# Performance work log

Hardware: AMD Instinct MI355X
Metric: run time of the kernel (lower is better)

Reference implementation:

```python
import jax, jax.numpy as jnp
import numpy as np

CONTINLEN = 5
ACCUMULATE_BETA = 50.0


def _triple_indices(n):
    """Flatten the module's triple loop into static gather indices over pairs.

    Pairs (a,b), a<b, are stored at flat index pair_id[(a,b)] along axis 0 of
    rotas/transs. For every (i,k,j) with i<k<j we need pairs (i,k), (k,j), (i,j).
    """
    pair_id = {}
    p = 0
    for a in range(n):
        for b in range(a + 1, n):
            pair_id[(a, b)] = p
            p += 1
    i1, i2, i12 = [], [], []
    for i in range(n):
        for j in range(i + 2, n):
            for k in range(i + 1, j):
                i1.append(pair_id[(i, k)])
                i2.append(pair_id[(k, j)])
                i12.append(pair_id[(i, j)])
    return (np.asarray(i1, np.int32), np.asarray(i2, np.int32),
            np.asarray(i12, np.int32))


def setup_inputs() -> dict:
    key = jax.random.key(0)
    k1, k2 = jax.random.split(key)
    P = CONTINLEN * (CONTINLEN - 1) // 2  # 10 ordered pairs
    B = 262144                              # batch of pose predictions
    rotas = jax.random.normal(k1, (P, B, 3, 3), dtype=jnp.float32)
    transs = jax.random.normal(k2, (P, B, 3), dtype=jnp.float32)
    return {"rotas": rotas, "transs": transs}


def reference(rotas, transs):
    i1, i2, i12 = _triple_indices(CONTINLEN)
    # Gather all (i,k), (k,j), (i,j) pose pairs at once: [T, B, 3, 3] / [T, B, 3]
    R1, R2, R12 = rotas[i1], rotas[i2], rotas[i12]
    t1, t2, t12 = transs[i1], transs[i2], transs[i12]
    # fuse_rota = R(i,k) @ R(k,j); fuse_trans = R(i,k) @ t(i,k) + t(k,j)
    fuse_rota = jnp.einsum('tbij,tbjk->tbik', R1, R2)
    fuse_trans = jnp.einsum('tbij,tbj->tbi', R1, t1) + t2
    rotaloss = jnp.sum(jnp.square(fuse_rota - R12))
    transloss = jnp.sum(jnp.square(fuse_trans - t12))
    return (rotaloss * ACCUMULATE_BETA + transloss).reshape(1)
```

## Files before the change

kernel.cpp:

```cpp
#include <hip/hip_runtime.h>

#define NPAIR 10
#define NTRI  10

__device__ __constant__ const int c_i1[NTRI]  = {0,0,1,0,1,2,4,4,5,7};
__device__ __constant__ const int c_i2[NTRI]  = {4,5,7,6,8,9,7,8,9,9};
__device__ __constant__ const int c_i12[NTRI] = {1,2,2,3,3,3,5,6,6,8};

__global__ __launch_bounds__(256) void accum_loss_kernel(
    const float* __restrict__ rotas,
    const float* __restrict__ transs,
    float* __restrict__ block_sums,
    int B)
{
    const int b = blockIdx.x * blockDim.x + threadIdx.x;

    float loss = 0.0f;
    if (b < B) {
        float R[NPAIR][9];
        float t[NPAIR][3];
#pragma unroll
        for (int p = 0; p < NPAIR; ++p) {
            const float* rp = rotas + ((size_t)p * B + b) * 9;
#pragma unroll
            for (int k = 0; k < 9; ++k) R[p][k] = rp[k];
            const float* tp = transs + ((size_t)p * B + b) * 3;
#pragma unroll
            for (int k = 0; k < 3; ++k) t[p][k] = tp[k];
        }

        float rl = 0.0f, tl = 0.0f;
#pragma unroll
        for (int tr = 0; tr < NTRI; ++tr) {
            const float* R1  = R[c_i1[tr]];
            const float* R2  = R[c_i2[tr]];
            const float* R12 = R[c_i12[tr]];
            const float* t1  = t[c_i1[tr]];
            const float* t2  = t[c_i2[tr]];
            const float* t12 = t[c_i12[tr]];
#pragma unroll
            for (int i = 0; i < 3; ++i) {
#pragma unroll
                for (int j = 0; j < 3; ++j) {
                    float f = fmaf(R1[i*3+0], R2[0*3+j],
                              fmaf(R1[i*3+1], R2[1*3+j],
                                   R1[i*3+2] * R2[2*3+j]));
                    float d = f - R12[i*3+j];
                    rl = fmaf(d, d, rl);
                }
                float ft = fmaf(R1[i*3+0], t1[0],
                           fmaf(R1[i*3+1], t1[1],
                                R1[i*3+2] * t1[2])) + t2[i];
                float dt = ft - t12[i];
                tl = fmaf(dt, dt, tl);
            }
        }
        loss = fmaf(rl, 50.0f, tl);
    }

#pragma unroll
    for (int off = 32; off >= 1; off >>= 1)
        loss += __shfl_down(loss, off, 64);

    __shared__ float ws[4];
    const int lane = threadIdx.x & 63;
    const int wid  = threadIdx.x >> 6;
    if (lane == 0) ws[wid] = loss;
    __syncthreads();
    if (threadIdx.x == 0)
        block_sums[blockIdx.x] = ws[0] + ws[1] + ws[2] + ws[3];
}

__global__ __launch_bounds__(256) void final_reduce_kernel(
    const float* __restrict__ block_sums, float* __restrict__ out, int n)
{
    float s = 0.0f;
    for (int i = threadIdx.x; i < n; i += blockDim.x) s += block_sums[i];
#pragma unroll
    for (int off = 32; off >= 1; off >>= 1)
        s += __shfl_down(s, off, 64);

    __shared__ float ws[4];
    const int lane = threadIdx.x & 63;
    const int wid  = threadIdx.x >> 6;
    if (lane == 0) ws[wid] = s;
    __syncthreads();
    if (threadIdx.x == 0)
        out[0] = ws[0] + ws[1] + ws[2] + ws[3];
}

extern "C" void kernel_launch(void* const* d_in, const int* in_sizes, int n_in,
                              void* d_out, int out_size, void* d_ws, size_t ws_size,
                              hipStream_t stream)
{
    const float* rotas  = (const float*)d_in[0];
    const float* transs = (const float*)d_in[1];
    float* out = (float*)d_out;

    const int B = in_sizes[0] / (NPAIR * 9);
    const int threads = 256;
    const int blocks  = (B + threads - 1) / threads;

    float* block_sums = (float*)d_ws;

    accum_loss_kernel<<<blocks, threads, 0, stream>>>(rotas, transs, block_sums, B);
    final_reduce_kernel<<<1, threads, 0, stream>>>(block_sums, out, blocks);
}
```

Before: 163.1 us.

## Stage pose loads through LDS for coalesced access with register prefetch

Each wave now loads each pair's rotation and translation data as contiguous 64-lane coalesced chunks, transposes them through per-wave double-buffered LDS into per-thread registers, and prefetches the next pair's global data while the current one is being redistributed. This replaces strided per-thread 36-byte and 12-byte loads that gave poor coalescing. The index tables become constexpr, and the bounds check is dropped on the assumption that B is a multiple of 256. If B is not a multiple of 256, the tail elements would be skipped.

```diff
diff --git a/kernel.cpp b/kernel.cpp
--- a/kernel.cpp
+++ b/kernel.cpp
@@ -3,9 +3,14 @@
 #define NPAIR 10
 #define NTRI  10
 
-__device__ __constant__ const int c_i1[NTRI]  = {0,0,1,0,1,2,4,4,5,7};
-__device__ __constant__ const int c_i2[NTRI]  = {4,5,7,6,8,9,7,8,9,9};
-__device__ __constant__ const int c_i12[NTRI] = {1,2,2,3,3,3,5,6,6,8};
+constexpr int c_i1[NTRI]  = {0,0,1,0,1,2,4,4,5,7};
+constexpr int c_i2[NTRI]  = {4,5,7,6,8,9,7,8,9,9};
+constexpr int c_i12[NTRI] = {1,2,2,3,3,3,5,6,6,8};
+
+#define LDS_FENCE() do {                      \
+    __builtin_amdgcn_s_waitcnt(0xC07F);       \
+    __builtin_amdgcn_wave_barrier();          \
+} while (0)
 
 __global__ __launch_bounds__(256) void accum_loss_kernel(
     const float* __restrict__ rotas,
@@ -13,61 +18,91 @@
     float* __restrict__ block_sums,
     int B)
 {
-    const int b = blockIdx.x * blockDim.x + threadIdx.x;
+    const int tid  = threadIdx.x;
+    const int lane = tid & 63;
+    const int wave = tid >> 6;
 
-    float loss = 0.0f;
-    if (b < B) {
-        float R[NPAIR][9];
-        float t[NPAIR][3];
+    __shared__ float sR[2][4][576];
+    __shared__ float sT[2][4][192];
+
+    const int wb0 = blockIdx.x * 256 + wave * 64;
+
+    float R[NPAIR][9];
+    float t[NPAIR][3];
+    float gR[9], gT[3];
+
+    {
+        const float* rsrc = rotas  + ((size_t)0 * B + wb0) * 9;
+        const float* tsrc = transs + ((size_t)0 * B + wb0) * 3;
 #pragma unroll
-        for (int p = 0; p < NPAIR; ++p) {
-            const float* rp = rotas + ((size_t)p * B + b) * 9;
+        for (int k = 0; k < 9; ++k) gR[k] = rsrc[k * 64 + lane];
 #pragma unroll
-            for (int k = 0; k < 9; ++k) R[p][k] = rp[k];
-            const float* tp = transs + ((size_t)p * B + b) * 3;
+        for (int k = 0; k < 3; ++k) gT[k] = tsrc[k * 64 + lane];
+    }
+
 #pragma unroll
-            for (int k = 0; k < 3; ++k) t[p][k] = tp[k];
+    for (int p = 0; p < NPAIR; ++p) {
+        const int buf = p & 1;
+#pragma unroll
+        for (int k = 0; k < 9; ++k) sR[buf][wave][k * 64 + lane] = gR[k];
+#pragma unroll
+        for (int k = 0; k < 3; ++k) sT[buf][wave][k * 64 + lane] = gT[k];
+
+        LDS_FENCE();
+
+        if (p + 1 < NPAIR) {
+            const float* rsrc = rotas  + ((size_t)(p + 1) * B + wb0) * 9;
+            const float* tsrc = transs + ((size_t)(p + 1) * B + wb0) * 3;
+#pragma unroll
+            for (int k = 0; k < 9; ++k) gR[k] = rsrc[k * 64 + lane];
+#pragma unroll
+            for (int k = 0; k < 3; ++k) gT[k] = tsrc[k * 64 + lane];
         }
 
-        float rl = 0.0f, tl = 0.0f;
 #pragma unroll
-        for (int tr = 0; tr < NTRI; ++tr) {
-            const float* R1  = R[c_i1[tr]];
-            const float* R2  = R[c_i2[tr]];
-            const float* R12 = R[c_i12[tr]];
-            const float* t1  = t[c_i1[tr]];
-            const float* t2  = t[c_i2[tr]];
-            const float* t12 = t[c_i12[tr]];
+        for (int k = 0; k < 9; ++k) R[p][k] = sR[buf][wave][lane * 9 + k];
 #pragma unroll
-            for (int i = 0; i < 3; ++i) {
+        for (int k = 0; k < 3; ++k) t[p][k] = sT[buf][wave][lane * 3 + k];
+
+        LDS_FENCE();
+    }
+
+    float rl = 0.0f, tl = 0.0f;
 #pragma unroll
-                for (int j = 0; j < 3; ++j) {
-                    float f = fmaf(R1[i*3+0], R2[0*3+j],
-                              fmaf(R1[i*3+1], R2[1*3+j],
-                                   R1[i*3+2] * R2[2*3+j]));
-                    float d = f - R12[i*3+j];
-                    rl = fmaf(d, d, rl);
-                }
-                float ft = fmaf(R1[i*3+0], t1[0],
-                           fmaf(R1[i*3+1], t1[1],
-                                R1[i*3+2] * t1[2])) + t2[i];
-                float dt = ft - t12[i];
-                tl = fmaf(dt, dt, tl);
+    for (int tr = 0; tr < NTRI; ++tr) {
+        const float* R1  = R[c_i1[tr]];
+        const float* R2  = R[c_i2[tr]];
+        const float* R12 = R[c_i12[tr]];
+        const float* t1  = t[c_i1[tr]];
+        const float* t2  = t[c_i2[tr]];
+        const float* t12 = t[c_i12[tr]];
+#pragma unroll
+        for (int i = 0; i < 3; ++i) {
+#pragma unroll
+            for (int j = 0; j < 3; ++j) {
+                float f = fmaf(R1[i*3+0], R2[0*3+j],
+                          fmaf(R1[i*3+1], R2[1*3+j],
+                               R1[i*3+2] * R2[2*3+j]));
+                float d = f - R12[i*3+j];
+                rl = fmaf(d, d, rl);
             }
+            float ft = fmaf(R1[i*3+0], t1[0],
+                       fmaf(R1[i*3+1], t1[1],
+                            R1[i*3+2] * t1[2])) + t2[i];
+            float dt = ft - t12[i];
+            tl = fmaf(dt, dt, tl);
         }
-        loss = fmaf(rl, 50.0f, tl);
     }
+    float loss = fmaf(rl, 50.0f, tl);
 
 #pragma unroll
     for (int off = 32; off >= 1; off >>= 1)
         loss += __shfl_down(loss, off, 64);
 
     __shared__ float ws[4];
-    const int lane = threadIdx.x & 63;
-    const int wid  = threadIdx.x >> 6;
-    if (lane == 0) ws[wid] = loss;
+    if (lane == 0) ws[wave] = loss;
     __syncthreads();
-    if (threadIdx.x == 0)
+    if (tid == 0)
         block_sums[blockIdx.x] = ws[0] + ws[1] + ws[2] + ws[3];
 }
 
@@ -99,7 +134,7 @@
 
     const int B = in_sizes[0] / (NPAIR * 9);
     const int threads = 256;
-    const int blocks  = (B + threads - 1) / threads;
+    const int blocks  = B / threads;
 
     float* block_sums = (float*)d_ws;
 
```

Measured after the change: 162.8 us. No clear change (-0.2%).
